# Optimization experiments

Hardware: AMD Instinct MI355X
Metric: run time of the kernel (lower is better)

## Reference

```python
import jax, jax.numpy as jnp
import numpy as np

B, S, H = 1, 2048, 2048
QL, KVL = 1536, 512
NH, NOPE, ROPE, VD = 16, 128, 64, 128
IH, ID = 16, 128
TOPK = 512
EPS = 1e-6


def _rms_norm(x, g):
    return x * jax.lax.rsqrt(jnp.mean(x * x, -1, keepdims=True) + EPS) * g


def _layer_norm(x, g, b):
    m = jnp.mean(x, -1, keepdims=True)
    v = jnp.mean((x - m) ** 2, -1, keepdims=True)
    return (x - m) * jax.lax.rsqrt(v + EPS) * g + b


def _rope(x, cos, sin):
    # x: [B,S,h,D] (D even), cos/sin: [S,D//2]; neox-style rotate-halves
    x1, x2 = jnp.split(x, 2, -1)
    c = cos[None, :, None, :]
    s = sin[None, :, None, :]
    return jnp.concatenate([x1 * c - x2 * s, x1 * s + x2 * c], -1)


def setup_inputs() -> dict:
    key = jax.random.key(0)
    ks = jax.random.split(key, 10)
    rn = lambda k, sh: (jax.random.normal(k, sh) * 0.02).astype(jnp.float32)
    pos = jnp.arange(S, dtype=jnp.float32)
    inv = 1.0 / (10000.0 ** (jnp.arange(0, ROPE, 2, dtype=jnp.float32) / ROPE))
    ang = pos[:, None] * inv[None, :]  # [S, ROPE//2]
    return {
        "hidden_states": jax.random.normal(ks[0], (B, S, H), jnp.float32),
        "cos": jnp.cos(ang),
        "sin": jnp.sin(ang),
        "Wq_a": rn(ks[1], (H, QL)),
        "q_a_gamma": jnp.ones((QL,), jnp.float32),
        "Wq_b": rn(ks[2], (QL, NH * (NOPE + ROPE))),
        "Wkv_a": rn(ks[3], (H, KVL + ROPE)),
        "kv_a_gamma": jnp.ones((KVL,), jnp.float32),
        "Wkv_b": rn(ks[4], (KVL, NH * (NOPE + VD))),
        "Wo": rn(ks[5], (NH * VD, H)),
        "Wq_idx": rn(ks[6], (QL, IH * ID)),
        "Wk_idx": rn(ks[7], (H, ID)),
        "Ww_idx": rn(ks[8], (H, IH)),
        "kn_gamma": jnp.ones((ID,), jnp.float32),
        "kn_beta": jnp.zeros((ID,), jnp.float32),
        "topk": TOPK,
    }


def reference(hidden_states, cos, sin, Wq_a, q_a_gamma, Wq_b, Wkv_a, kv_a_gamma,
              Wkv_b, Wo, Wq_idx, Wk_idx, Ww_idx, kn_gamma, kn_beta, topk):
    b, s, _ = hidden_states.shape
    softmax_scale = (NOPE + ROPE) ** -0.5

    # ---- low-rank Q path ----
    q_a = _rms_norm(hidden_states @ Wq_a, q_a_gamma)                 # [B,S,QL]
    q = (q_a @ Wq_b).reshape(b, s, NH, NOPE + ROPE)
    q_nope, q_pe = q[..., :NOPE], _rope(q[..., NOPE:], cos, sin)

    # ---- latent KV path (MQA rope key) ----
    kv = hidden_states @ Wkv_a                                        # [B,S,KVL+ROPE]
    kv_c = _rms_norm(kv[..., :KVL], kv_a_gamma)
    k_pe = _rope(kv[..., KVL:][:, :, None, :], cos, sin)[:, :, 0]     # [B,S,ROPE]
    kvb = (kv_c @ Wkv_b).reshape(b, s, NH, NOPE + VD)
    k_nope, v = kvb[..., :NOPE], kvb[..., NOPE:]

    # ---- lightning indexer: I[t,s] = sum_h w[t,h] * relu(q_idx[t,h] . k_idx[s]) ----
    qi = (q_a @ Wq_idx).reshape(b, s, IH, ID)
    qi = jnp.concatenate([_rope(qi[..., :ROPE], cos, sin), qi[..., ROPE:]], -1)
    ki = _layer_norm(hidden_states @ Wk_idx, kn_gamma, kn_beta)       # [B,S,ID]
    ki = jnp.concatenate([_rope(ki[:, :, None, :ROPE], cos, sin)[:, :, 0], ki[..., ROPE:]], -1)
    w = hidden_states @ Ww_idx                                        # [B,S,IH]
    s_h = jax.nn.relu(jnp.einsum('bthd,bsd->bhts', qi, ki)) * (ID ** -0.5)
    idx_scores = jnp.einsum('bth,bhts->bts', w, s_h)                  # [B,S,S]

    causal = jnp.tril(jnp.ones((s, s), bool))
    idx_scores = jnp.where(causal[None], idx_scores, -jnp.inf)
    top_idx = jax.lax.top_k(idx_scores, topk)[1]                      # [B,S,topk]
    sel = jnp.zeros((b, s, s), bool).at[
        jnp.arange(b)[:, None, None], jnp.arange(s)[None, :, None], top_idx
    ].set(True)
    mask = sel & causal[None]                                         # [B,S,S]

    # ---- sparse MLA attention over selected tokens ----
    scores = (jnp.einsum('bthd,bshd->bhts', q_nope, k_nope)
              + jnp.einsum('bthd,bsd->bhts', q_pe, k_pe)) * softmax_scale
    scores = jnp.where(mask[:, None], scores, -jnp.inf)
    attn = jax.nn.softmax(scores, -1)                                 # [B,NH,S,S]
    out = jnp.einsum('bhts,bshd->bthd', attn, v).reshape(b, s, NH * VD)
    return out @ Wo                                                   # [B,S,H]
```

## Files before the change

kernel.cpp:

```cpp
#include <hip/hip_runtime.h>
#include <cstdint>
#include <cstddef>
#include <cmath>

typedef unsigned long long u64;
typedef __attribute__((ext_vector_type(8))) short bf16x8;
typedef __attribute__((ext_vector_type(4))) float f32x4;

static constexpr int S_    = 2048;
static constexpr int H_    = 2048;
static constexpr int TOPKC = 512;

#define SCALE_ATTN 0.07216878364870323f
#define ISCALE_ID  0.08838834764831845f
#define EPS_F 1e-6f

__device__ inline unsigned short f2b(float f) {
  unsigned u = __float_as_uint(f);
  return (unsigned short)((u + 0x7FFFu + ((u >> 16) & 1u)) >> 16);
}
__device__ inline float b2f(unsigned short b) {
  return __uint_as_float(((unsigned)b) << 16);
}
__device__ inline void gload16(const unsigned short* g, unsigned short* l) {
  __builtin_amdgcn_global_load_lds((const __attribute__((address_space(1))) void*)g,
                                   (__attribute__((address_space(3))) void*)l, 16, 0, 0);
}

template<int MODE>
__global__ __launch_bounds__(256) void k_gemm_bf16(
    const unsigned short* __restrict__ A, int lda,
    const unsigned short* __restrict__ Bt, int K,
    void* __restrict__ C, int ldc, int N,
    const float* __restrict__ cosb, const float* __restrict__ sinb) {
  __shared__ unsigned short As[128 * 64];
  __shared__ unsigned short Bs[128 * 64];
  int nwg = gridDim.x * gridDim.y;
  int orig = blockIdx.y * gridDim.x + blockIdx.x;
  int q = nwg >> 3, r = nwg & 7;
  int xcd = orig & 7, sub = orig >> 3;
  int wgid = (xcd < r ? xcd * (q + 1) : r * (q + 1) + (xcd - r) * q) + sub;
  int by = wgid / gridDim.x, bx = wgid - by * gridDim.x;
  const int bm = by * 128, bn = bx * 128;
  const int tid = threadIdx.x;
  const int lane = tid & 63, w = tid >> 6;
  const int wm = w >> 1, wn = w & 1;
  const int l15 = lane & 15, quarter = lane >> 4;
  const int srow = (lane >> 3), scol = (lane & 7) * 8;

  f32x4 acc[4][4];
#pragma unroll
  for (int i = 0; i < 4; i++)
#pragma unroll
    for (int j = 0; j < 4; j++) acc[i][j] = (f32x4){0.f, 0.f, 0.f, 0.f};

  for (int k0 = 0; k0 < K; k0 += 64) {
    __syncthreads();
#pragma unroll
    for (int i = 0; i < 4; i++) {
      int r0 = w * 32 + i * 8;
      gload16(A  + (size_t)(bm + r0 + srow) * lda + k0 + scol, &As[r0 * 64]);
      gload16(Bt + (size_t)(bn + r0 + srow) * K   + k0 + scol, &Bs[r0 * 64]);
    }
    __syncthreads();
#pragma unroll
    for (int kc = 0; kc < 2; kc++) {
      bf16x8 af[4], bfr[4];
#pragma unroll
      for (int mf = 0; mf < 4; mf++)
        af[mf] = *(const bf16x8*)(As + (wm * 64 + mf * 16 + l15) * 64 + kc * 32 + quarter * 8);
#pragma unroll
      for (int nf = 0; nf < 4; nf++)
        bfr[nf] = *(const bf16x8*)(Bs + (wn * 64 + nf * 16 + l15) * 64 + kc * 32 + quarter * 8);
#pragma unroll
      for (int mf = 0; mf < 4; mf++)
#pragma unroll
        for (int nf = 0; nf < 4; nf++)
          acc[mf][nf] = __builtin_amdgcn_mfma_f32_16x16x32_bf16(af[mf], bfr[nf], acc[mf][nf], 0, 0, 0);
    }
  }
  if constexpr (MODE == 2) {
    if (bn >= 3072 && wn == 0) {
#pragma unroll
      for (int mf = 0; mf < 4; mf++)
#pragma unroll
        for (int r2 = 0; r2 < 4; r2++) {
          int t = bm + wm * 64 + mf * 16 + quarter * 4 + r2;
#pragma unroll
          for (int nf = 0; nf < 2; nf++) {
            int i = nf * 16 + l15;
            float c = cosb[t * 32 + i], s = sinb[t * 32 + i];
            float x1 = acc[mf][nf][r2], x2 = acc[mf][nf + 2][r2];
            acc[mf][nf][r2]     = x1 * c - x2 * s;
            acc[mf][nf + 2][r2] = x1 * s + x2 * c;
          }
        }
    }
  }
#pragma unroll
  for (int mf = 0; mf < 4; mf++)
#pragma unroll
    for (int nf = 0; nf < 4; nf++)
#pragma unroll
      for (int r2 = 0; r2 < 4; r2++) {
        int grow = bm + wm * 64 + mf * 16 + quarter * 4 + r2;
        int gcol = bn + wn * 64 + nf * 16 + l15;
        if (gcol < N) {
          if constexpr (MODE != 0) ((unsigned short*)C)[(size_t)grow * ldc + gcol] = f2b(acc[mf][nf][r2]);
          else                     ((float*)C)[(size_t)grow * ldc + gcol] = acc[mf][nf][r2];
        }
      }
}

__device__ inline void tcast_tile(const float* __restrict__ W, int K, int N,
                                  unsigned short* __restrict__ dst,
                                  int r, int ntx, int tid, float (*T)[33]) {
  int xt = r % ntx, kt = r / ntx;
  int n0 = xt * 32, k0 = kt * 32;
#pragma unroll
  for (int i = 0; i < 4; i++) {
    int idx = tid + 256 * i;
    int rr = idx >> 5, c = idx & 31;
    T[rr][c] = W[(size_t)(k0 + rr) * N + n0 + c];
  }
  __syncthreads();
#pragma unroll
  for (int i = 0; i < 4; i++) {
    int idx = tid + 256 * i;
    int rr = idx >> 5, c = idx & 31;
    dst[(size_t)(n0 + rr) * K + k0 + c] = f2b(T[c][rr]);
  }
}

__global__ __launch_bounds__(256) void k_tcast_p1(
    const float* __restrict__ Wq_a, const float* __restrict__ Wkv_a,
    const float* __restrict__ Wk_idx, const float* __restrict__ Ww_idx,
    const float* __restrict__ hs, unsigned short* __restrict__ hs_b,
    unsigned short* __restrict__ WT) {
  __shared__ float T[32][33];
  int bid = blockIdx.x, tid = threadIdx.x;
  if (bid < 3072)      tcast_tile(Wq_a,  2048, 1536, WT,                          bid,        48, tid, T);
  else if (bid < 4224) tcast_tile(Wkv_a, 2048,  576, WT + (size_t)1536 * 2048,    bid - 3072, 18, tid, T);
  else if (bid < 4480) tcast_tile(Wk_idx,2048,  128, WT + (size_t)2112 * 2048,    bid - 4224,  4, tid, T);
  else if (bid < 4608) {
    int idx = (bid - 4480) * 256 + tid;
    int k = idx >> 4, n = idx & 15;
    WT[(size_t)(2240 + n) * 2048 + k] = f2b(Ww_idx[(size_t)k * 16 + n]);
  } else {
    int idx = ((bid - 4608) * 256 + tid) * 4;
    const float* ip = hs + idx;
    unsigned short* op = hs_b + idx;
    op[0] = f2b(ip[0]); op[1] = f2b(ip[1]); op[2] = f2b(ip[2]); op[3] = f2b(ip[3]);
  }
}

__global__ __launch_bounds__(256) void k_tcast_p2(
    const float* __restrict__ Wq_b, const float* __restrict__ Wq_idx,
    unsigned short* __restrict__ WT) {
  __shared__ float T[32][33];
  int bid = blockIdx.x, tid = threadIdx.x;
  if (bid < 4608) tcast_tile(Wq_b,   1536, 3072, WT,                        bid,        96, tid, T);
  else            tcast_tile(Wq_idx, 1536, 2048, WT + (size_t)3072 * 1536,  bid - 4608, 64, tid, T);
}

__global__ __launch_bounds__(256) void k_tcast_p3(
    const float* __restrict__ Wkv_b, const float* __restrict__ Wo,
    unsigned short* __restrict__ WT) {
  __shared__ float T[32][33];
  int bid = blockIdx.x, tid = threadIdx.x;
  if (bid < 2048) tcast_tile(Wkv_b,  512, 4096, WT,                       bid,        128, tid, T);
  else            tcast_tile(Wo,    2048, 2048, WT + (size_t)4096 * 512,  bid - 2048,  64, tid, T);
}

__global__ __launch_bounds__(256) void k_norms(
    const float* __restrict__ fat, int stride,
    const float* __restrict__ qg, const float* __restrict__ kvg,
    const float* __restrict__ kng, const float* __restrict__ knb,
    const float* __restrict__ cosb, const float* __restrict__ sinb,
    unsigned short* __restrict__ qa_b, unsigned short* __restrict__ kvc_b,
    unsigned short* __restrict__ kpe_b, unsigned short* __restrict__ ki_b) {
  int t = blockIdx.x, tid = threadIdx.x;
  const float* p = fat + (size_t)t * stride;
  __shared__ float red[256];
  __shared__ float buf[128];
  float x[6]; float s = 0.f;
#pragma unroll
  for (int i = 0; i < 6; i++) { x[i] = p[tid + 256 * i]; s += x[i] * x[i]; }
  red[tid] = s; __syncthreads();
  for (int st = 128; st > 0; st >>= 1) { if (tid < st) red[tid] += red[tid + st]; __syncthreads(); }
  float scl = rsqrtf(red[0] * (1.f / 1536.f) + EPS_F);
#pragma unroll
  for (int i = 0; i < 6; i++)
    qa_b[(size_t)t * 1536 + tid + 256 * i] = f2b(x[i] * scl * qg[tid + 256 * i]);
  __syncthreads();
  float y0 = p[1536 + tid], y1 = p[1792 + tid];
  red[tid] = y0 * y0 + y1 * y1; __syncthreads();
  for (int st = 128; st > 0; st >>= 1) { if (tid < st) red[tid] += red[tid + st]; __syncthreads(); }
  float scl2 = rsqrtf(red[0] * (1.f / 512.f) + EPS_F);
  kvc_b[(size_t)t * 512 + tid]       = f2b(y0 * scl2 * kvg[tid]);
  kvc_b[(size_t)t * 512 + 256 + tid] = f2b(y1 * scl2 * kvg[256 + tid]);
  if (tid < 32) {
    float a = p[2048 + tid], b = p[2080 + tid];
    float c = cosb[t * 32 + tid], sn = sinb[t * 32 + tid];
    kpe_b[(size_t)t * 64 + tid]      = f2b(a * c - b * sn);
    kpe_b[(size_t)t * 64 + 32 + tid] = f2b(a * sn + b * c);
  }
  __syncthreads();
  float z = (tid < 128) ? p[2112 + tid] : 0.f;
  red[tid] = z; __syncthreads();
  for (int st = 128; st > 0; st >>= 1) { if (tid < st) red[tid] += red[tid + st]; __syncthreads(); }
  float mean = red[0] * (1.f / 128.f);
  __syncthreads();
  float d = (tid < 128) ? (z - mean) : 0.f;
  red[tid] = d * d; __syncthreads();
  for (int st = 128; st > 0; st >>= 1) { if (tid < st) red[tid] += red[tid + st]; __syncthreads(); }
  float var = red[0] * (1.f / 128.f);
  if (tid < 128) buf[tid] = d * rsqrtf(var + EPS_F) * kng[tid] + knb[tid];
  __syncthreads();
  if (tid < 128) {
    float outv;
    if (tid < 32) {
      float c = cosb[t * 32 + tid], sn = sinb[t * 32 + tid];
      outv = buf[tid] * c - buf[tid + 32] * sn;
    } else if (tid < 64) {
      int j = tid - 32;
      float c = cosb[t * 32 + j], sn = sinb[t * 32 + j];
      outv = buf[j] * sn + buf[tid] * c;
    } else outv = buf[tid];
    ki_b[(size_t)t * 128 + tid] = f2b(outv);
  }
}

__global__ __launch_bounds__(256) void k_idx_mfma(
    const unsigned short* __restrict__ qi_b, int qpitch,
    const unsigned short* __restrict__ ki_b,
    const float* __restrict__ wb, int wstride,
    float* __restrict__ out) {
  int bid = blockIdx.x;
  int tb = (int)((sqrtf(8.f * bid + 1.f) - 1.f) * 0.5f);
  while ((tb + 1) * (tb + 2) / 2 <= bid) tb++;
  while (tb * (tb + 1) / 2 > bid) tb--;
  int sb = bid - tb * (tb + 1) / 2;
  int t0 = tb * 64, s0 = sb * 64;

  int tid = threadIdx.x, lane = tid & 63, w = tid >> 6;
  int wm = w >> 1, wn = w & 1;
  int l15 = lane & 15, quarter = lane >> 4;

  __shared__ unsigned short Ks[64 * 128];
  __shared__ unsigned short Qs[2][64 * 128];
  __shared__ float Ws[64][16];

  int srow_[4], scc_[4];
#pragma unroll
  for (int i = 0; i < 4; i++) {
    int row = w * 16 + i * 4 + (lane >> 4);
    srow_[i] = row;
    scc_[i] = (lane & 15) ^ (row & 7);
  }
#pragma unroll
  for (int i = 0; i < 4; i++) {
    gload16(ki_b + (size_t)(s0 + srow_[i]) * 128 + scc_[i] * 8, &Ks[(w * 16 + i * 4) * 128]);
    gload16(qi_b + (size_t)(t0 + srow_[i]) * qpitch + scc_[i] * 8, &Qs[0][(w * 16 + i * 4) * 128]);
  }
  for (int i = tid; i < 64 * 16; i += 256) Ws[i >> 4][i & 15] = wb[(size_t)(t0 + (i >> 4)) * wstride + (i & 15)];
  __syncthreads();

  bf16x8 bfr[2][4];
#pragma unroll
  for (int nf = 0; nf < 2; nf++) {
    int row = wn * 32 + nf * 16 + l15;
    int rx = (row & 7) << 3;
#pragma unroll
    for (int kc = 0; kc < 4; kc++)
      bfr[nf][kc] = *(const bf16x8*)(Ks + row * 128 + ((kc * 32 + quarter * 8) ^ rx));
  }

  f32x4 acc[2][2];
#pragma unroll
  for (int mf = 0; mf < 2; mf++)
#pragma unroll
    for (int nf = 0; nf < 2; nf++) acc[mf][nf] = (f32x4){0.f, 0.f, 0.f, 0.f};

  for (int h = 0; h < 16; h++) {
    int cur = h & 1;
    if (h < 15) {
#pragma unroll
      for (int i = 0; i < 4; i++)
        gload16(qi_b + (size_t)(t0 + srow_[i]) * qpitch + (h + 1) * 128 + scc_[i] * 8,
                &Qs[cur ^ 1][(w * 16 + i * 4) * 128]);
    }
    f32x4 acch[2][2];
#pragma unroll
    for (int mf = 0; mf < 2; mf++)
#pragma unroll
      for (int nf = 0; nf < 2; nf++) acch[mf][nf] = (f32x4){0.f, 0.f, 0.f, 0.f};

    __builtin_amdgcn_s_setprio(1);
#pragma unroll
    for (int mf = 0; mf < 2; mf++) {
      int row = wm * 32 + mf * 16 + l15;
      int rx = (row & 7) << 3;
      bf16x8 af[4];
#pragma unroll
      for (int kc = 0; kc < 4; kc++)
        af[kc] = *(const bf16x8*)(Qs[cur] + row * 128 + ((kc * 32 + quarter * 8) ^ rx));
#pragma unroll
      for (int nf = 0; nf < 2; nf++)
#pragma unroll
        for (int kc = 0; kc < 4; kc++)
          acch[mf][nf] = __builtin_amdgcn_mfma_f32_16x16x32_bf16(af[kc], bfr[nf][kc], acch[mf][nf], 0, 0, 0);
    }
    __builtin_amdgcn_s_setprio(0);
#pragma unroll
    for (int mf = 0; mf < 2; mf++) {
#pragma unroll
      for (int r = 0; r < 4; r++) {
        float wv = Ws[wm * 32 + mf * 16 + quarter * 4 + r][h];
#pragma unroll
        for (int nf = 0; nf < 2; nf++)
          acc[mf][nf][r] = fmaf(wv, fmaxf(acch[mf][nf][r], 0.f), acc[mf][nf][r]);
      }
    }
    __syncthreads();
  }
#pragma unroll
  for (int mf = 0; mf < 2; mf++)
#pragma unroll
    for (int nf = 0; nf < 2; nf++)
#pragma unroll
      for (int r = 0; r < 4; r++) {
        int t = t0 + wm * 32 + mf * 16 + quarter * 4 + r;
        int s = s0 + wn * 32 + nf * 16 + l15;
        out[(size_t)t * 2048 + s] = acc[mf][nf][r] * ISCALE_ID;
      }
}

__global__ __launch_bounds__(256) void k_topk_mask(const float* __restrict__ idx_sc, u64* __restrict__ maskw) {
  int t = blockIdx.x;
  int tid = threadIdx.x;
  int n = t + 1;
  if (n <= TOPKC) {
    if (tid < 32) {
      int lo = tid * 64, hi = lo + 63;
      u64 wv;
      if (t >= hi) wv = ~0ULL;
      else if (t < lo) wv = 0ULL;
      else wv = (~0ULL) >> (63 - (t - lo));
      maskw[(size_t)t * 32 + tid] = wv;
    }
    return;
  }
  __shared__ unsigned int u[2048];
  __shared__ int hist[256];
  __shared__ int wtot[4];
  __shared__ u64 mw[32];
  __shared__ int sel_b, new_target;
  __shared__ int cnt[32];
  __shared__ u64 tmask[32];
  int lane = tid & 63, wid = tid >> 6;
  if (tid < 32) mw[tid] = 0ULL;
  const float* row = idx_sc + (size_t)t * 2048;
  for (int s = tid; s < n; s += 256) {
    unsigned int bb = __float_as_uint(row[s]);
    u[s] = (bb & 0x80000000u) ? ~bb : (bb | 0x80000000u);
  }
  unsigned int prefix = 0;
  int target = TOPKC;
  for (int shift = 24; shift >= 0; shift -= 8) {
    hist[tid] = 0;
    __syncthreads();
    unsigned int himask = (shift == 24) ? 0u : (0xFFFFFFFFu << (shift + 8));
    for (int s = tid; s < n; s += 256) {
      unsigned int uv = u[s];
      if ((uv & himask) == prefix) atomicAdd(&hist[(uv >> shift) & 0xFF], 1);
    }
    __syncthreads();
    int h = hist[tid];
    int sum = h;
#pragma unroll
    for (int off = 1; off < 64; off <<= 1) {
      int tv = __shfl_down(sum, off);
      if (lane + off < 64) sum += tv;
    }
    if (lane == 0) wtot[wid] = sum;
    __syncthreads();
    int scan = sum;
    for (int wI = wid + 1; wI < 4; wI++) scan += wtot[wI];
    if (scan >= target && scan - h < target) {
      sel_b = tid;
      new_target = target - (scan - h);
    }
    __syncthreads();
    prefix |= ((unsigned int)sel_b) << shift;
    target = new_target;
  }
#pragma unroll
  for (int i = 0; i < 8; i++) {
    int s = i * 256 + tid;
    bool in = (s < n);
    unsigned int uv = in ? u[s] : 0u;
    bool tie = in && (uv == prefix);
    u64 bal = __ballot(tie);
    if (lane == 0) { int c = i * 4 + wid; cnt[c] = __popcll(bal); tmask[c] = bal; }
    if (in && uv > prefix) atomicOr(&mw[s >> 6], 1ULL << (s & 63));
  }
  __syncthreads();
#pragma unroll
  for (int i = 0; i < 8; i++) {
    int s = i * 256 + tid;
    if (s >= n) continue;
    if (u[s] != prefix) continue;
    int c = i * 4 + wid;
    int base = 0;
    for (int c2 = 0; c2 < c; c2++) base += cnt[c2];
    int rank = base + __popcll(tmask[c] & ((1ULL << lane) - 1ULL));
    if (rank < target) atomicOr(&mw[s >> 6], 1ULL << (s & 63));
  }
  __syncthreads();
  if (tid < 32) maskw[(size_t)t * 32 + tid] = mw[tid];
}

__global__ __launch_bounds__(256) void k_attn_mfma(
    const unsigned short* __restrict__ qb, int qpitch,
    const unsigned short* __restrict__ kvb_b,
    const unsigned short* __restrict__ kpe_b,
    const float* __restrict__ cosb, const float* __restrict__ sinb,
    const u64* __restrict__ maskw,
    unsigned short* __restrict__ attn_b) {
  int ybm = blockIdx.x;
  int h = blockIdx.y;
  int yb = (h < 8) ? ybm : (31 - ybm);
  int t0 = yb * 64;
  int tid = threadIdx.x;
  int lane = tid & 63, wq = tid >> 6;
  int quarter = lane >> 4, l15 = lane & 15;

  __shared__ unsigned short Kd[2][64 * 192];
  __shared__ unsigned short Vts[128 * 64];

  const unsigned short* kb_base[6];
  int kb_step[6];
#pragma unroll
  for (int i = 0; i < 6; i++) {
    int slot = (wq * 6 + i) * 1024 + lane * 16;
    int rowk = slot / 384;
    int coff = slot - rowk * 384;
    int cc = (coff ^ ((rowk & 7) << 4)) >> 4;
    if (cc < 16) { kb_base[i] = kvb_b + (size_t)rowk * 4096 + h * 256 + cc * 8; kb_step[i] = 4096; }
    else         { kb_base[i] = kpe_b + (size_t)rowk * 64 + (cc - 16) * 8;      kb_step[i] = 64; }
  }
  const int vdg = tid & 15, vsp = tid >> 4;
  const unsigned short* vbase = kvb_b + (size_t)(vsp * 4) * 4096 + h * 256 + 128 + vdg * 8;

  bf16x8 qf[6];
  {
    int t = t0 + wq * 16 + l15;
    const unsigned short* qp = qb + (size_t)t * qpitch + h * 192 + quarter * 8;
#pragma unroll
    for (int kc = 0; kc < 6; kc++) qf[kc] = *(const bf16x8*)(qp + kc * 32);
    const float* cp = cosb + t * 32 + quarter * 8;
    const float* sp = sinb + t * 32 + quarter * 8;
    float4 ca = *(const float4*)cp,  cb2 = *(const float4*)(cp + 4);
    float4 sa = *(const float4*)sp,  sb2 = *(const float4*)(sp + 4);
    float carr[8] = {ca.x, ca.y, ca.z, ca.w, cb2.x, cb2.y, cb2.z, cb2.w};
    float sarr[8] = {sa.x, sa.y, sa.z, sa.w, sb2.x, sb2.y, sb2.z, sb2.w};
#pragma unroll
    for (int j = 0; j < 8; j++) {
      float x1 = b2f((unsigned short)qf[4][j]);
      float x2 = b2f((unsigned short)qf[5][j]);
      qf[4][j] = (short)f2b(x1 * carr[j] - x2 * sarr[j]);
      qf[5][j] = (short)f2b(x1 * sarr[j] + x2 * carr[j]);
    }
  }

  f32x4 o[8];
#pragma unroll
  for (int df = 0; df < 8; df++) o[df] = (f32x4){0.f, 0.f, 0.f, 0.f};
  float mcol = -__builtin_inff(), lcol = 0.f;
  const u64* mrow = maskw + (size_t)(t0 + wq * 16 + l15) * 32;
  int nsb = yb + 1;

#pragma unroll
  for (int i = 0; i < 6; i++) gload16(kb_base[i], &Kd[0][(wq * 6 + i) * 512]);
  bf16x8 vr0 = *(const bf16x8*)(vbase);
  bf16x8 vr1 = *(const bf16x8*)(vbase + 4096);
  bf16x8 vr2 = *(const bf16x8*)(vbase + 8192);
  bf16x8 vr3 = *(const bf16x8*)(vbase + 12288);
  __syncthreads();
#pragma unroll
  for (int j = 0; j < 8; j++) {
    int d = vdg * 8 + j;
    uint2 w2;
    w2.x = (unsigned)(unsigned short)vr0[j] | (((unsigned)(unsigned short)vr1[j]) << 16);
    w2.y = (unsigned)(unsigned short)vr2[j] | (((unsigned)(unsigned short)vr3[j]) << 16);
    *(uint2*)((char*)Vts + d * 128 + ((vsp * 8) ^ (((d >> 2) & 7) << 4))) = w2;
  }

  for (int sb = 0; sb < nsb; sb++) {
    int cur = sb & 1;
    __syncthreads();
    bool pf = (sb + 1 < nsb);
    if (pf) {
      size_t sn = (size_t)(sb + 1) * 64;
#pragma unroll
      for (int i = 0; i < 6; i++)
        gload16(kb_base[i] + sn * kb_step[i], &Kd[cur ^ 1][(wq * 6 + i) * 512]);
      const unsigned short* vp = vbase + sn * 4096;
      vr0 = *(const bf16x8*)(vp);
      vr1 = *(const bf16x8*)(vp + 4096);
      vr2 = *(const bf16x8*)(vp + 8192);
      vr3 = *(const bf16x8*)(vp + 12288);
    }
    const unsigned short* Kc = Kd[cur];
    f32x4 sfT[4];
#pragma unroll
    for (int sc = 0; sc < 4; sc++) {
      f32x4 a = (f32x4){0.f, 0.f, 0.f, 0.f};
      int row = sc * 16 + l15;
      int rx = (row & 7) << 4;
#pragma unroll
      for (int kc = 0; kc < 6; kc++) {
        int byte = row * 384 + ((kc * 64 + quarter * 16) ^ rx);
        bf16x8 kf = *(const bf16x8*)((const char*)Kc + byte);
        a = __builtin_amdgcn_mfma_f32_16x16x32_bf16(kf, qf[kc], a, 0, 0, 0);
      }
      sfT[sc] = a;
    }
    u64 w64 = mrow[sb];
    float p[4][4];
#pragma unroll
    for (int sc = 0; sc < 4; sc++)
#pragma unroll
      for (int r = 0; r < 4; r++) {
        int sbit = sc * 16 + quarter * 4 + r;
        bool sel = (w64 >> sbit) & 1ULL;
        p[sc][r] = sel ? sfT[sc][r] * SCALE_ATTN : -__builtin_inff();
      }
    float v = p[0][0];
#pragma unroll
    for (int sc = 0; sc < 4; sc++)
#pragma unroll
      for (int r = 0; r < 4; r++) v = fmaxf(v, p[sc][r]);
    v = fmaxf(v, __shfl_xor(v, 16));
    v = fmaxf(v, __shfl_xor(v, 32));
    float mn = fmaxf(mcol, v);
    bool dead = (mn == -__builtin_inff());
    float scl = dead ? 1.f : __expf(mcol - mn);
#pragma unroll
    for (int sc = 0; sc < 4; sc++)
#pragma unroll
      for (int r = 0; r < 4; r++)
        p[sc][r] = dead ? 0.f : __expf(p[sc][r] - mn);
    mcol = dead ? mcol : mn;
    float rs = 0.f;
#pragma unroll
    for (int sc = 0; sc < 4; sc++)
#pragma unroll
      for (int r = 0; r < 4; r++) rs += p[sc][r];
    rs += __shfl_xor(rs, 16);
    rs += __shfl_xor(rs, 32);
    lcol = lcol * scl + rs;

    unsigned pk[4][2];
#pragma unroll
    for (int sc = 0; sc < 4; sc++)
#pragma unroll
      for (int rr = 0; rr < 2; rr++)
        pk[sc][rr] = (unsigned)f2b(p[sc][2 * rr]) | (((unsigned)f2b(p[sc][2 * rr + 1])) << 16);
    bf16x8 pa[2];
#pragma unroll
    for (int kc = 0; kc < 2; kc++) {
      union { unsigned d[4]; bf16x8 v; } pu;
#pragma unroll
      for (int jj = 0; jj < 4; jj++) {
        int src = ((quarter & 1) * 2 + (jj >> 1)) * 16 + l15;
        unsigned lo = (unsigned)__shfl((int)pk[kc * 2][jj & 1], src);
        unsigned hi = (unsigned)__shfl((int)pk[kc * 2 + 1][jj & 1], src);
        pu.d[jj] = (quarter < 2) ? lo : hi;
      }
      pa[kc] = pu.v;
    }
    float sclr[4];
#pragma unroll
    for (int r = 0; r < 4; r++) sclr[r] = __shfl(scl, quarter * 4 + r);
#pragma unroll
    for (int df = 0; df < 8; df++)
#pragma unroll
      for (int r = 0; r < 4; r++) o[df][r] *= sclr[r];
#pragma unroll
    for (int kc = 0; kc < 2; kc++)
#pragma unroll
      for (int df = 0; df < 8; df++) {
        int d = df * 16 + l15;
        int vbyte = d * 128 + ((kc * 64 + quarter * 16) ^ (((d >> 2) & 7) << 4));
        bf16x8 vf = *(const bf16x8*)((const char*)Vts + vbyte);
        o[df] = __builtin_amdgcn_mfma_f32_16x16x32_bf16(pa[kc], vf, o[df], 0, 0, 0);
      }
    __syncthreads();
    if (pf) {
#pragma unroll
      for (int j = 0; j < 8; j++) {
        int d = vdg * 8 + j;
        uint2 w2;
        w2.x = (unsigned)(unsigned short)vr0[j] | (((unsigned)(unsigned short)vr1[j]) << 16);
        w2.y = (unsigned)(unsigned short)vr2[j] | (((unsigned)(unsigned short)vr3[j]) << 16);
        *(uint2*)((char*)Vts + d * 128 + ((vsp * 8) ^ (((d >> 2) & 7) << 4))) = w2;
      }
    }
  }
  float inv = (lcol > 0.f) ? 1.f / lcol : 0.f;
  float invr[4];
#pragma unroll
  for (int r = 0; r < 4; r++) invr[r] = __shfl(inv, quarter * 4 + r);
#pragma unroll
  for (int r = 0; r < 4; r++) {
    int t = t0 + wq * 16 + quarter * 4 + r;
    unsigned short* op = attn_b + (size_t)t * 2048 + h * 128 + l15;
#pragma unroll
    for (int df = 0; df < 8; df++) op[df * 16] = f2b(o[df][r] * invr[r]);
  }
}

extern "C" void kernel_launch(void* const* d_in, const int* in_sizes, int n_in,
                              void* d_out, int out_size, void* d_ws, size_t ws_size,
                              hipStream_t stream) {
  const float* hs     = (const float*)d_in[0];
  const float* cosb   = (const float*)d_in[1];
  const float* sinb   = (const float*)d_in[2];
  const float* Wq_a   = (const float*)d_in[3];
  const float* q_a_g  = (const float*)d_in[4];
  const float* Wq_b   = (const float*)d_in[5];
  const float* Wkv_a  = (const float*)d_in[6];
  const float* kv_a_g = (const float*)d_in[7];
  const float* Wkv_b  = (const float*)d_in[8];
  const float* Wo     = (const float*)d_in[9];
  const float* Wq_idx = (const float*)d_in[10];
  const float* Wk_idx = (const float*)d_in[11];
  const float* Ww_idx = (const float*)d_in[12];
  const float* kn_g   = (const float*)d_in[13];
  const float* kn_b   = (const float*)d_in[14];
  float* out = (float*)d_out;

  char* base = (char*)d_ws;
  size_t off = 0;
  auto alloc = [&](size_t bytes) { void* p = base + off; off += (bytes + 255) & ~size_t(255); return p; };

  float* fat1 = (float*)alloc((size_t)S_ * 2304 * 4);
  unsigned short* attn_b = (unsigned short*)fat1;
  float* idxs = (float*)alloc((size_t)S_ * 2048 * 4);
  unsigned short* fat2 = (unsigned short*)alloc((size_t)S_ * 5120 * 2);
  u64*   maskw = (u64*)alloc((size_t)S_ * 32 * 8);
  unsigned short* hs_b  = (unsigned short*)alloc((size_t)S_ * 2048 * 2);
  unsigned short* qa_b  = (unsigned short*)alloc((size_t)S_ * 1536 * 2);
  unsigned short* kvc_b = (unsigned short*)alloc((size_t)S_ * 512 * 2);
  unsigned short* kpe_b = (unsigned short*)alloc((size_t)S_ * 64 * 2);
  unsigned short* kvb_b = (unsigned short*)alloc((size_t)S_ * 4096 * 2);
  unsigned short* ki_b  = (unsigned short*)alloc((size_t)S_ * 128 * 2);
  unsigned short* WT    = (unsigned short*)alloc((size_t)5120 * 1536 * 2);

  dim3 blk(256);

  k_tcast_p1<<<dim3(8704), blk, 0, stream>>>(Wq_a, Wkv_a, Wk_idx, Ww_idx, hs, hs_b, WT);
  k_gemm_bf16<0><<<dim3(18, 16), blk, 0, stream>>>(hs_b, 2048, WT, 2048, fat1, 2304, 2256, nullptr, nullptr);
  k_norms<<<dim3(S_), blk, 0, stream>>>(fat1, 2304, q_a_g, kv_a_g, kn_g, kn_b, cosb, sinb,
                                        qa_b, kvc_b, kpe_b, ki_b);
  k_tcast_p2<<<dim3(7680), blk, 0, stream>>>(Wq_b, Wq_idx, WT);
  k_gemm_bf16<2><<<dim3(40, 16), blk, 0, stream>>>(qa_b, 1536, WT, 1536, fat2, 5120, 5120, cosb, sinb);
  k_tcast_p3<<<dim3(6144), blk, 0, stream>>>(Wkv_b, Wo, WT);
  k_gemm_bf16<1><<<dim3(32, 16), blk, 0, stream>>>(kvc_b, 512, WT, 512, kvb_b, 4096, 4096, nullptr, nullptr);
  k_idx_mfma<<<dim3(528), blk, 0, stream>>>(fat2 + 3072, 5120, ki_b, fat1 + 2240, 2304, idxs);
  k_topk_mask<<<dim3(S_), blk, 0, stream>>>(idxs, maskw);
  k_attn_mfma<<<dim3(32, 16), blk, 0, stream>>>(fat2, 5120, kvb_b, kpe_b, cosb, sinb, maskw, attn_b);
  k_gemm_bf16<0><<<dim3(16, 16), blk, 0, stream>>>(attn_b, 2048, WT + (size_t)4096 * 512, 2048, out, 2048, 2048, nullptr, nullptr);

  (void)in_sizes; (void)n_in; (void)out_size; (void)ws_size;
}
```

Measured before the change: 345.2 us.

## Merge first two weight-cast kernels and use 128x64-tile GEMM with XCD remap

Fuses the first two transpose-cast launches into one kernel. Because the cast weights for the first GEMM would otherwise overwrite the region needed by the second, they now live in the idxs scratch buffer. Adds a GEMM variant with 128x64 tiles and an XCD-aware workgroup remap, used for the two fp32-output GEMMs, which are the only ones with small grids (288 and 256 blocks). The aim is to cut launch overhead and fill more CUs, at the cost of less reuse per tile.

```diff
diff --git a/kernel.cpp b/kernel.cpp
--- a/kernel.cpp
+++ b/kernel.cpp
@@ -105,10 +105,73 @@
       for (int r2 = 0; r2 < 4; r2++) {
         int grow = bm + wm * 64 + mf * 16 + quarter * 4 + r2;
         int gcol = bn + wn * 64 + nf * 16 + l15;
-        if (gcol < N) {
-          if constexpr (MODE != 0) ((unsigned short*)C)[(size_t)grow * ldc + gcol] = f2b(acc[mf][nf][r2]);
-          else                     ((float*)C)[(size_t)grow * ldc + gcol] = acc[mf][nf][r2];
-        }
+        if (gcol < N)
+          ((unsigned short*)C)[(size_t)grow * ldc + gcol] = f2b(acc[mf][nf][r2]);
+      }
+}
+
+__global__ __launch_bounds__(256) void k_gemm_n64(
+    const unsigned short* __restrict__ A, int lda,
+    const unsigned short* __restrict__ Bt, int K,
+    float* __restrict__ C, int ldc, int N) {
+  __shared__ unsigned short As[128 * 64];
+  __shared__ unsigned short Bs[64 * 64];
+  int nwg = gridDim.x * gridDim.y;
+  int orig = blockIdx.y * gridDim.x + blockIdx.x;
+  int q = nwg >> 3, r = nwg & 7;
+  int xcd = orig & 7, sub = orig >> 3;
+  int wgid = (xcd < r ? xcd * (q + 1) : r * (q + 1) + (xcd - r) * q) + sub;
+  int by = wgid / gridDim.x, bx = wgid - by * gridDim.x;
+  const int bm = by * 128, bn = bx * 64;
+  const int tid = threadIdx.x;
+  const int lane = tid & 63, w = tid >> 6;
+  const int l15 = lane & 15, quarter = lane >> 4;
+  const int srow = (lane >> 3), scol = (lane & 7) * 8;
+
+  f32x4 acc[2][4];
+#pragma unroll
+  for (int i = 0; i < 2; i++)
+#pragma unroll
+    for (int j = 0; j < 4; j++) acc[i][j] = (f32x4){0.f, 0.f, 0.f, 0.f};
+
+  for (int k0 = 0; k0 < K; k0 += 64) {
+    __syncthreads();
+#pragma unroll
+    for (int i = 0; i < 4; i++) {
+      int r0 = w * 32 + i * 8;
+      gload16(A + (size_t)(bm + r0 + srow) * lda + k0 + scol, &As[r0 * 64]);
+    }
+#pragma unroll
+    for (int i = 0; i < 2; i++) {
+      int r0 = w * 16 + i * 8;
+      gload16(Bt + (size_t)(bn + r0 + srow) * K + k0 + scol, &Bs[r0 * 64]);
+    }
+    __syncthreads();
+#pragma unroll
+    for (int kc = 0; kc < 2; kc++) {
+      bf16x8 af[2], bfr[4];
+#pragma unroll
+      for (int mf = 0; mf < 2; mf++)
+        af[mf] = *(const bf16x8*)(As + (w * 32 + mf * 16 + l15) * 64 + kc * 32 + quarter * 8);
+#pragma unroll
+      for (int nf = 0; nf < 4; nf++)
+        bfr[nf] = *(const bf16x8*)(Bs + (nf * 16 + l15) * 64 + kc * 32 + quarter * 8);
+#pragma unroll
+      for (int mf = 0; mf < 2; mf++)
+#pragma unroll
+        for (int nf = 0; nf < 4; nf++)
+          acc[mf][nf] = __builtin_amdgcn_mfma_f32_16x16x32_bf16(af[mf], bfr[nf], acc[mf][nf], 0, 0, 0);
+    }
+  }
+#pragma unroll
+  for (int mf = 0; mf < 2; mf++)
+#pragma unroll
+    for (int nf = 0; nf < 4; nf++)
+#pragma unroll
+      for (int r2 = 0; r2 < 4; r2++) {
+        int grow = bm + w * 32 + mf * 16 + quarter * 4 + r2;
+        int gcol = bn + nf * 16 + l15;
+        if (gcol < N) C[(size_t)grow * ldc + gcol] = acc[mf][nf][r2];
       }
 }
 
@@ -132,35 +195,30 @@
   }
 }
 
-__global__ __launch_bounds__(256) void k_tcast_p1(
+__global__ __launch_bounds__(256) void k_tcast_p12(
     const float* __restrict__ Wq_a, const float* __restrict__ Wkv_a,
     const float* __restrict__ Wk_idx, const float* __restrict__ Ww_idx,
     const float* __restrict__ hs, unsigned short* __restrict__ hs_b,
-    unsigned short* __restrict__ WT) {
+    unsigned short* __restrict__ WT1,
+    const float* __restrict__ Wq_b, const float* __restrict__ Wq_idx,
+    unsigned short* __restrict__ WT2) {
   __shared__ float T[32][33];
   int bid = blockIdx.x, tid = threadIdx.x;
-  if (bid < 3072)      tcast_tile(Wq_a,  2048, 1536, WT,                          bid,        48, tid, T);
-  else if (bid < 4224) tcast_tile(Wkv_a, 2048,  576, WT + (size_t)1536 * 2048,    bid - 3072, 18, tid, T);
-  else if (bid < 4480) tcast_tile(Wk_idx,2048,  128, WT + (size_t)2112 * 2048,    bid - 4224,  4, tid, T);
+  if (bid < 3072)       tcast_tile(Wq_a,  2048, 1536, WT1,                        bid,         48, tid, T);
+  else if (bid < 4224)  tcast_tile(Wkv_a, 2048,  576, WT1 + (size_t)1536 * 2048,  bid - 3072,  18, tid, T);
+  else if (bid < 4480)  tcast_tile(Wk_idx,2048,  128, WT1 + (size_t)2112 * 2048,  bid - 4224,   4, tid, T);
   else if (bid < 4608) {
     int idx = (bid - 4480) * 256 + tid;
     int k = idx >> 4, n = idx & 15;
-    WT[(size_t)(2240 + n) * 2048 + k] = f2b(Ww_idx[(size_t)k * 16 + n]);
-  } else {
+    WT1[(size_t)(2240 + n) * 2048 + k] = f2b(Ww_idx[(size_t)k * 16 + n]);
+  } else if (bid < 8704) {
     int idx = ((bid - 4608) * 256 + tid) * 4;
     const float* ip = hs + idx;
     unsigned short* op = hs_b + idx;
     op[0] = f2b(ip[0]); op[1] = f2b(ip[1]); op[2] = f2b(ip[2]); op[3] = f2b(ip[3]);
   }
-}
-
-__global__ __launch_bounds__(256) void k_tcast_p2(
-    const float* __restrict__ Wq_b, const float* __restrict__ Wq_idx,
-    unsigned short* __restrict__ WT) {
-  __shared__ float T[32][33];
-  int bid = blockIdx.x, tid = threadIdx.x;
-  if (bid < 4608) tcast_tile(Wq_b,   1536, 3072, WT,                        bid,        96, tid, T);
-  else            tcast_tile(Wq_idx, 1536, 2048, WT + (size_t)3072 * 1536,  bid - 4608, 64, tid, T);
+  else if (bid < 13312) tcast_tile(Wq_b,   1536, 3072, WT2,                        bid - 8704,  96, tid, T);
+  else                  tcast_tile(Wq_idx, 1536, 2048, WT2 + (size_t)3072 * 1536,  bid - 13312, 64, tid, T);
 }
 
 __global__ __launch_bounds__(256) void k_tcast_p3(
@@ -649,6 +707,7 @@
   float* fat1 = (float*)alloc((size_t)S_ * 2304 * 4);
   unsigned short* attn_b = (unsigned short*)fat1;
   float* idxs = (float*)alloc((size_t)S_ * 2048 * 4);
+  unsigned short* WT1 = (unsigned short*)idxs;
   unsigned short* fat2 = (unsigned short*)alloc((size_t)S_ * 5120 * 2);
   u64*   maskw = (u64*)alloc((size_t)S_ * 32 * 8);
   unsigned short* hs_b  = (unsigned short*)alloc((size_t)S_ * 2048 * 2);
@@ -661,18 +720,18 @@
 
   dim3 blk(256);
 
-  k_tcast_p1<<<dim3(8704), blk, 0, stream>>>(Wq_a, Wkv_a, Wk_idx, Ww_idx, hs, hs_b, WT);
-  k_gemm_bf16<0><<<dim3(18, 16), blk, 0, stream>>>(hs_b, 2048, WT, 2048, fat1, 2304, 2256, nullptr, nullptr);
+  k_tcast_p12<<<dim3(16384), blk, 0, stream>>>(Wq_a, Wkv_a, Wk_idx, Ww_idx, hs, hs_b, WT1,
+                                               Wq_b, Wq_idx, WT);
+  k_gemm_n64<<<dim3(36, 16), blk, 0, stream>>>(hs_b, 2048, WT1, 2048, fat1, 2304, 2256);
   k_norms<<<dim3(S_), blk, 0, stream>>>(fat1, 2304, q_a_g, kv_a_g, kn_g, kn_b, cosb, sinb,
                                         qa_b, kvc_b, kpe_b, ki_b);
-  k_tcast_p2<<<dim3(7680), blk, 0, stream>>>(Wq_b, Wq_idx, WT);
   k_gemm_bf16<2><<<dim3(40, 16), blk, 0, stream>>>(qa_b, 1536, WT, 1536, fat2, 5120, 5120, cosb, sinb);
   k_tcast_p3<<<dim3(6144), blk, 0, stream>>>(Wkv_b, Wo, WT);
   k_gemm_bf16<1><<<dim3(32, 16), blk, 0, stream>>>(kvc_b, 512, WT, 512, kvb_b, 4096, 4096, nullptr, nullptr);
   k_idx_mfma<<<dim3(528), blk, 0, stream>>>(fat2 + 3072, 5120, ki_b, fat1 + 2240, 2304, idxs);
   k_topk_mask<<<dim3(S_), blk, 0, stream>>>(idxs, maskw);
   k_attn_mfma<<<dim3(32, 16), blk, 0, stream>>>(fat2, 5120, kvb_b, kpe_b, cosb, sinb, maskw, attn_b);
-  k_gemm_bf16<0><<<dim3(16, 16), blk, 0, stream>>>(attn_b, 2048, WT + (size_t)4096 * 512, 2048, out, 2048, 2048, nullptr, nullptr);
+  k_gemm_n64<<<dim3(32, 16), blk, 0, stream>>>(attn_b, 2048, WT + (size_t)4096 * 512, 2048, out, 2048, 2048);
 
   (void)in_sizes; (void)n_in; (void)out_size; (void)ws_size;
 }
```

New measurement: 337.2 us. 2.3% less time.
